# Optimization experiments

Hardware: AMD Instinct MI355X
Metric: run time of the kernel (lower is better)

## Reference

```python
import jax, jax.numpy as jnp
import numpy as np
from jax.scipy.linalg import expm

S = 64          # alphabet size (codons)
M = 8           # number of models, prod(model_shape)
N_LEAVES = 32   # leaves of the balanced binary tree
N_EDGES = 62    # nodes 0..62, every non-root node has one parent edge (edge id == child node id)
B = 1024        # batch (alignment columns)
# per-level ranges of child-node ids; node 32+j has children (2j, 2j+1), etc.
LEVELS = [(0, 32), (32, 48), (48, 56), (56, 60), (60, 62)]


def inv_stereographic_projection(p):
    # maps R^{s-1} -> unit sphere S^{s-1}
    n2 = jnp.sum(p * p, axis=-1, keepdims=True)
    return jnp.concatenate([2.0 * p / (n2 + 1.0), (n2 - 1.0) / (n2 + 1.0)], axis=-1)


def generator(R, pi):
    # R: (M, s(s-1)/2) exchangeabilities, pi: (M, s) stationary distribution
    iu, ju = np.triu_indices(S, 1)
    A = jnp.zeros((M, S, S), R.dtype).at[:, iu, ju].set(R).at[:, ju, iu].set(R)
    Q = A * pi[:, None, :]                       # Q_ij = A_ij * pi_j (off-diagonal)
    row = jnp.sum(Q, axis=-1)                    # (M, S)
    return Q - jnp.eye(S, dtype=Q.dtype) * row[:, :, None]


def felsenstein(leave_configuration, R_inv, pi_inv, lengths):
    pi = inv_stereographic_projection(pi_inv) ** 2           # (M, S), rows sum to 1
    R = jnp.exp(R_inv)                                       # positive rates
    Q = generator(R, pi)                                     # (M, S, S)
    tQ = lengths[:, None, None, None] * Q[None]              # (E, M, S, S)
    P = jax.vmap(expm)(tQ.reshape(-1, S, S)).reshape(N_EDGES, M, S, S)
    # leaf alphas: tile leaf observations over the M models -> (n_leaves, B, M, S)
    prev = jnp.broadcast_to(
        leave_configuration.transpose(1, 0, 2)[:, :, None, :],
        (N_LEAVES, leave_configuration.shape[0], M, S))
    # level-synchronous pruning: messages up each parent edge, then product of the two children
    for a, b in LEVELS:
        msg = jnp.einsum('emcd,ebmd->ebmc', P[a:b], prev)    # per-edge transition
        prev = msg[0::2] * msg[1::2]                         # combine sibling pairs
    root = prev[0]                                           # (B, M, S)
    out = jnp.einsum('bms,ms->bm', root, pi)                 # P(data | model m)
    return out.reshape(out.shape[0], M)                      # (B, *model_shape)


def setup_inputs() -> dict:
    key = jax.random.key(0)
    k1, k2, k3, k4 = jax.random.split(key, 4)
    leave_configuration = jax.random.uniform(k1, (B, N_LEAVES, S), dtype=jnp.float32)
    tree_indices = jnp.zeros((B,), dtype=jnp.int32)          # single tree (F=1)
    R_inv = jax.random.uniform(k2, (M, S * (S - 1) // 2), dtype=jnp.float32,
                               minval=-1.0, maxval=1.0)
    pi_inv = jnp.full((M, S - 1), 1.0 / (np.sqrt(S) - 1.0), dtype=jnp.float32) \
        + 0.01 * jax.random.normal(k3, (M, S - 1), dtype=jnp.float32)
    lengths = jax.random.uniform(k4, (N_EDGES,), dtype=jnp.float32,
                                 minval=0.05, maxval=0.5)
    return {'leave_configuration': leave_configuration, 'R_inv': R_inv,
            'pi_inv': pi_inv, 'lengths': lengths, 'tree_indices': tree_indices}


def reference(leave_configuration, R_inv, pi_inv, lengths, tree_indices):
    # F=1: tf.dynamic_partition/gather_nd batch slicing is the identity, so
    # tree_indices is closed over / unused.
    return felsenstein(leave_configuration, R_inv, pi_inv, lengths)
```

## Files before the change

kernel.cpp:

```cpp
#include <hip/hip_runtime.h>

typedef unsigned short u16;
typedef unsigned int u32;
typedef __attribute__((ext_vector_type(8))) __bf16 bf16x8;
typedef __attribute__((ext_vector_type(4))) float f32x4;

constexpr size_t OFF_PI  = 0;
constexpr size_t OFF_PBH = 512;
constexpr size_t OFF_PBL = OFF_PBH + 1015808;

union FR { uint4 u; bf16x8 v; };

__device__ __forceinline__ void split_bf16(float x, u16& h, u16& l) {
  u32 b = __float_as_uint(x);
  u32 hb = (b + 0x7fffu + ((b >> 16) & 1u)) & 0xffff0000u;
  h = (u16)(hb >> 16);
  float r = x - __uint_as_float(hb);
  l = (u16)(__float_as_uint(r) >> 16);
}

__device__ __forceinline__ void split8(const f32x4 a, const f32x4 b,
                                       uint4& hi, uint4& lo) {
  u16 h[8], l[8];
  split_bf16(a.x, h[0], l[0]); split_bf16(a.y, h[1], l[1]);
  split_bf16(a.z, h[2], l[2]); split_bf16(a.w, h[3], l[3]);
  split_bf16(b.x, h[4], l[4]); split_bf16(b.y, h[5], l[5]);
  split_bf16(b.z, h[6], l[6]); split_bf16(b.w, h[7], l[7]);
  hi.x = h[0] | ((u32)h[1] << 16); hi.y = h[2] | ((u32)h[3] << 16);
  hi.z = h[4] | ((u32)h[5] << 16); hi.w = h[6] | ((u32)h[7] << 16);
  lo.x = l[0] | ((u32)l[1] << 16); lo.y = l[2] | ((u32)l[3] << 16);
  lo.z = l[4] | ((u32)l[5] << 16); lo.w = l[6] | ((u32)l[7] << 16);
}

__device__ __forceinline__ void mfma3(f32x4& a, const uint4 ah, const uint4 al,
                                      const uint4 bh, const uint4 bl) {
  FR Ah, Al, Bh, Bl;
  Ah.u = ah; Al.u = al; Bh.u = bh; Bl.u = bl;
  a = __builtin_amdgcn_mfma_f32_16x16x32_bf16(Ah.v, Bh.v, a, 0, 0, 0);
  a = __builtin_amdgcn_mfma_f32_16x16x32_bf16(Ah.v, Bl.v, a, 0, 0, 0);
  a = __builtin_amdgcn_mfma_f32_16x16x32_bf16(Al.v, Bh.v, a, 0, 0, 0);
}

__device__ __forceinline__ void xt_read2(const u32* b, int row, int chunk,
                                         uint4& hi, uint4& lo) {
  const int dw = (row << 5) + (((chunk + row) & 7) << 2);
  hi = *(const uint4*)&b[dw];
  lo = *(const uint4*)&b[2048 + dw];
}
__device__ __forceinline__ void xt_write4(u32* b, int row, int cp, int half,
                                          const f32x4 v) {
  u16 h[4], l[4];
  split_bf16(v.x, h[0], l[0]); split_bf16(v.y, h[1], l[1]);
  split_bf16(v.z, h[2], l[2]); split_bf16(v.w, h[3], l[3]);
  const int dw = (row << 5) + (((cp + row) & 7) << 2) + half * 2;
  uint2 hh, ll;
  hh.x = h[0] | ((u32)h[1] << 16); hh.y = h[2] | ((u32)h[3] << 16);
  ll.x = l[0] | ((u32)l[1] << 16); ll.y = l[2] | ((u32)l[3] << 16);
  *(uint2*)&b[dw] = hh;
  *(uint2*)&b[2048 + dw] = ll;
}

__global__ __launch_bounds__(1024) void k_pcomb(
    const float* __restrict__ R_inv, const float* __restrict__ pi_inv,
    const float* __restrict__ lengths, float* __restrict__ ws,
    u16* __restrict__ PBH, u16* __restrict__ PBL) {
  const int m = blockIdx.x & 7, prt = blockIdx.x >> 3;
  const int tid = threadIdx.x, lane = tid & 63, w = tid >> 6;
  const int ln = lane & 15, kq = lane >> 4;
  const int ct = w >> 2, bt = w & 3;
  __shared__ float pis[64];
  __shared__ float n2s;
  __shared__ __align__(16) float Qs[64 * 68];
  __shared__ __align__(16) u32 PB[7][4096];

  if (tid < 64) {
    float p = (tid < 63) ? pi_inv[m * 63 + tid] : 0.f;
    float v = p * p;
    #pragma unroll
    for (int off = 32; off; off >>= 1) v += __shfl_down(v, off, 64);
    if (tid == 0) n2s = v;
  }
  __syncthreads();
  if (tid < 64) {
    const float den = n2s + 1.f;
    const float x = (tid < 63) ? 2.f * pi_inv[m * 63 + tid] / den
                               : (n2s - 1.f) / den;
    const float pv = x * x;
    pis[tid] = pv;
    if (prt == 0) ws[OFF_PI + (size_t)m * 64 + tid] = pv;
  }
  __syncthreads();
  for (int idx = tid; idx < 4096; idx += 1024) {
    const int i = idx >> 6, j = idx & 63;
    float q = 0.f;
    if (i != j) {
      const int a = min(i, j), b = max(i, j);
      const int kk = a * (127 - a) / 2 + (b - a - 1);
      q = expf(R_inv[m * 2016 + kk]) * pis[j];
    }
    Qs[i * 68 + j] = q;
  }
  __syncthreads();
  if (tid < 64) {
    float s = 0.f;
    #pragma unroll 4
    for (int j4 = 0; j4 < 64; j4 += 4) {
      const f32x4 q = *(const f32x4*)&Qs[tid * 68 + j4];
      s += q.x + q.y + q.z + q.w;
    }
    Qs[tid * 68 + tid] = -s;
  }
  __syncthreads();
  float q[12][4];
  #pragma unroll
  for (int r = 0; r < 4; ++r) q[0][r] = Qs[(ct * 16 + kq * 4 + r) * 68 + bt * 16 + ln];
  if (tid < 512) {
    const int i = tid >> 3, c = tid & 7;
    const f32x4 a = *(const f32x4*)&Qs[i * 68 + c * 8];
    const f32x4 b = *(const f32x4*)&Qs[i * 68 + c * 8 + 4];
    uint4 h, l;
    split8(a, b, h, l);
    const int dw = (i << 5) + (((c + i) & 7) << 2);
    *(uint4*)&PB[0][dw] = h;
    *(uint4*)&PB[0][2048 + dw] = l;
  } else {
    const int t2 = tid - 512, j = t2 >> 3, c = t2 & 7;
    f32x4 a, b;
    a.x = Qs[(c * 8 + 0) * 68 + j]; a.y = Qs[(c * 8 + 1) * 68 + j];
    a.z = Qs[(c * 8 + 2) * 68 + j]; a.w = Qs[(c * 8 + 3) * 68 + j];
    b.x = Qs[(c * 8 + 4) * 68 + j]; b.y = Qs[(c * 8 + 5) * 68 + j];
    b.z = Qs[(c * 8 + 6) * 68 + j]; b.w = Qs[(c * 8 + 7) * 68 + j];
    uint4 h, l;
    split8(a, b, h, l);
    const int dw = (j << 5) + (((c + j) & 7) << 2);
    *(uint4*)&PB[3][dw] = h;
    *(uint4*)&PB[3][2048 + dw] = l;
  }
  __syncthreads();

  const f32x4 z = {0.f, 0.f, 0.f, 0.f};
  auto mmstep = [&](const u32* RX, const u32* CY, float* qk, u32* dstC,
                    u32* dstR) {
    uint4 ah[2], al[2], bh[2], bl[2];
    #pragma unroll
    for (int kh = 0; kh < 2; ++kh) {
      xt_read2(RX, ct * 16 + ln, kh * 4 + kq, ah[kh], al[kh]);
      xt_read2(CY, bt * 16 + ln, kh * 4 + kq, bh[kh], bl[kh]);
    }
    f32x4 a = z;
    #pragma unroll
    for (int kh = 0; kh < 2; ++kh) mfma3(a, ah[kh], al[kh], bh[kh], bl[kh]);
    #pragma unroll
    for (int r = 0; r < 4; ++r) qk[r] = a[r];
    if (dstC) xt_write4(dstC, bt * 16 + ln, 2 * ct + (kq >> 1), kq & 1, a);
    if (dstR) {
      #pragma unroll
      for (int kh = 0; kh < 2; ++kh) {
        xt_read2(CY, ct * 16 + ln, kh * 4 + kq, ah[kh], al[kh]);
        xt_read2(RX, bt * 16 + ln, kh * 4 + kq, bh[kh], bl[kh]);
      }
      f32x4 a2 = z;
      #pragma unroll
      for (int kh = 0; kh < 2; ++kh) mfma3(a2, ah[kh], al[kh], bh[kh], bl[kh]);
      xt_write4(dstR, bt * 16 + ln, 2 * ct + (kq >> 1), kq & 1, a2);
    }
  };
  mmstep(PB[0], PB[3], q[1], PB[4], PB[1]);  __syncthreads();
  mmstep(PB[1], PB[3], q[2], PB[5], nullptr); __syncthreads();
  mmstep(PB[1], PB[4], q[3], PB[6], PB[2]);  __syncthreads();
  mmstep(PB[2], PB[3], q[4], nullptr, nullptr);
  mmstep(PB[2], PB[4], q[5], nullptr, nullptr);
  mmstep(PB[2], PB[5], q[6], nullptr, nullptr);
  mmstep(PB[2], PB[6], q[7], nullptr, PB[0]); __syncthreads();
  mmstep(PB[0], PB[3], q[8], nullptr, nullptr);
  mmstep(PB[0], PB[4], q[9], nullptr, nullptr);
  mmstep(PB[0], PB[5], q[10], nullptr, nullptr);
  mmstep(PB[0], PB[6], q[11], nullptr, nullptr);

  #pragma unroll
  for (int ei = 0; ei < 2; ++ei) {
    const int e = prt * 2 + ei;
    if (e >= 62) break;
    const float t = lengths[e];
    const int jcol = bt * 16 + ln;
    float av[4];
    #pragma unroll
    for (int r = 0; r < 4; ++r)
      av[r] = (ct * 16 + kq * 4 + r == jcol) ? 1.f : 0.f;
    float cf = 1.f;
    #pragma unroll
    for (int k = 1; k <= 12; ++k) {
      cf *= t / (float)k;
      #pragma unroll
      for (int r = 0; r < 4; ++r) av[r] = fmaf(cf, q[k - 1][r], av[r]);
    }
    const size_t base = (((size_t)e * 8 + m) << 12) + jcol;
    #pragma unroll
    for (int r = 0; r < 4; ++r) {
      u16 h, l;
      split_bf16(av[r], h, l);
      const size_t o = base + (size_t)(ct * 16 + kq * 4 + r) * 64;
      PBH[o] = h;
      PBL[o] = l;
    }
  }
}

#define SE(e, i0, i1, o) \
  ((u32)(e) | ((u32)(i0) << 8) | ((u32)(i1) << 16) | ((u32)(o) << 24))
__device__ const u32 SCHED[31] = {
    SE(0, 0, 0, 0),  SE(2, 0, 0, 1),  SE(4, 0, 0, 2),  SE(6, 0, 0, 3),
    SE(32, 0, 1, 4), SE(34, 2, 3, 5), SE(8, 0, 0, 6),  SE(10, 0, 0, 7),
    SE(36, 6, 7, 8), SE(12, 0, 0, 0), SE(14, 0, 0, 1), SE(16, 0, 0, 2),
    SE(38, 0, 1, 3), SE(48, 4, 5, 6), SE(18, 0, 0, 7),
    SE(40, 2, 7, 0), SE(50, 8, 3, 1), SE(20, 0, 0, 4), SE(22, 0, 0, 5),
    SE(42, 4, 5, 2), SE(24, 0, 0, 3), SE(26, 0, 0, 7), SE(56, 6, 1, 8),
    SE(52, 0, 2, 1), SE(44, 3, 7, 4), SE(28, 0, 0, 5), SE(30, 0, 0, 6),
    SE(46, 5, 6, 0),
    SE(54, 4, 0, 2),
    SE(58, 1, 2, 3),
    SE(60, 8, 3, 15)};
__device__ const int PH[12] = {0, 4, 8, 12, 15, 19, 23, 27, 28, 29, 30, 31};

__global__ __launch_bounds__(512, 4) void k_tree(
    const float* __restrict__ leaves, const u16* __restrict__ Phi,
    const u16* __restrict__ Plo, const float* __restrict__ ws,
    float* __restrict__ out) {
  const int m = blockIdx.x & 7, btile = blockIdx.x >> 3;
  const int tid = threadIdx.x, lane = tid & 63, w = tid >> 6;
  const int ln = lane & 15, kq = lane >> 4;
  const int ct0 = (w & 1) * 2;
  __shared__ __align__(16) u32 slots[9 * 2048];
  __shared__ float psum[2][4][16];
  const f32x4 z = {0.f, 0.f, 0.f, 0.f};
  f32x4 rootp[2][2] = {{z, z}, {z, z}};

  for (int ph = 0; ph < 11; ++ph) {
    const int p0 = PH[ph], np = PH[ph + 1] - p0;
    const int pi = w >> 1;
    if (pi < np) {
      const u32 d = SCHED[p0 + pi];
      const int e0 = d & 0xff, i0 = (d >> 8) & 0xff, i1 = (d >> 16) & 0xff,
                os = d >> 24;
      f32x4 acc[2][2];
      #pragma unroll
      for (int s = 0; s < 2; ++s) {
        uint4 bh[2][2], bl[2][2];
        if (e0 < 32) {
          #pragma unroll
          for (int bi = 0; bi < 2; ++bi) {
            const int row = bi * 16 + ln;
            #pragma unroll
            for (int kh = 0; kh < 2; ++kh) {
              const float* g = leaves + (size_t)(btile * 32 + row) * 2048 +
                               (size_t)(e0 + s) * 64 + kh * 32 + kq * 8;
              const f32x4 xa = *(const f32x4*)g;
              const f32x4 xb = *(const f32x4*)(g + 4);
              split8(xa, xb, bh[bi][kh], bl[bi][kh]);
            }
          }
        } else {
          const u32* nb0 = &slots[(s ? i1 : i0) * 2048];
          #pragma unroll
          for (int bi = 0; bi < 2; ++bi) {
            const int row = bi * 16 + ln;
            const u32* nb = nb0 + row * 64;
            #pragma unroll
            for (int kh = 0; kh < 2; ++kh) {
              const int jc = kh * 8 + kq * 2;
              const uint4 A = *(const uint4*)&nb[((jc + row) & 15) << 2];
              const uint4 B = *(const uint4*)&nb[((jc + 1 + row) & 15) << 2];
              bh[bi][kh].x = A.x; bh[bi][kh].y = A.y;
              bh[bi][kh].z = B.x; bh[bi][kh].w = B.y;
              bl[bi][kh].x = A.z; bl[bi][kh].y = A.w;
              bl[bi][kh].z = B.z; bl[bi][kh].w = B.w;
            }
          }
        }
        uint4 pfh[2][2], pfl[2][2];
        const size_t pb = ((size_t)(e0 + s) * 8 + m) << 12;
        #pragma unroll
        for (int ci = 0; ci < 2; ++ci)
          #pragma unroll
          for (int kh = 0; kh < 2; ++kh) {
            const size_t off =
                pb + (size_t)((ct0 + ci) * 16 + ln) * 64 + kh * 32 + kq * 8;
            pfh[ci][kh] = *(const uint4*)(Phi + off);
            pfl[ci][kh] = *(const uint4*)(Plo + off);
          }
        #pragma unroll
        for (int ci = 0; ci < 2; ++ci)
          #pragma unroll
          for (int bi = 0; bi < 2; ++bi) {
            f32x4 a = z;
            #pragma unroll
            for (int kh = 0; kh < 2; ++kh)
              mfma3(a, pfh[ci][kh], pfl[ci][kh], bh[bi][kh], bl[bi][kh]);
            if (s == 0) {
              acc[ci][bi] = a;
            } else {
              const f32x4 pr = acc[ci][bi] * a;
              if (os == 15) {
                rootp[ci][bi] = pr;
              } else {
                u16 h[4], l[4];
                split_bf16(pr.x, h[0], l[0]); split_bf16(pr.y, h[1], l[1]);
                split_bf16(pr.z, h[2], l[2]); split_bf16(pr.w, h[3], l[3]);
                uint4 pk;
                pk.x = h[0] | ((u32)h[1] << 16); pk.y = h[2] | ((u32)h[3] << 16);
                pk.z = l[0] | ((u32)l[1] << 16); pk.w = l[2] | ((u32)l[3] << 16);
                const int row = bi * 16 + ln;
                const int jc = (ct0 + ci) * 4 + kq;
                *(uint4*)&slots[os * 2048 + row * 64 +
                                (((jc + row) & 15) << 2)] = pk;
              }
            }
          }
      }
    }
    __syncthreads();
  }
  if (w < 2) {
    #pragma unroll
    for (int ci = 0; ci < 2; ++ci) {
      const int ct = ct0 + ci;
      const f32x4 piv =
          *(const f32x4*)&ws[OFF_PI + (size_t)m * 64 + ct * 16 + kq * 4];
      #pragma unroll
      for (int bi = 0; bi < 2; ++bi) {
        const f32x4 pr = rootp[ci][bi];
        float v = pr.x * piv.x + pr.y * piv.y + pr.z * piv.z + pr.w * piv.w;
        v += __shfl_xor(v, 16, 64);
        v += __shfl_xor(v, 32, 64);
        if (lane < 16) psum[bi][ct][lane] = v;
      }
    }
  }
  __syncthreads();
  if (tid < 32) {
    const int bi = tid >> 4, bb = tid & 15;
    out[(size_t)(btile * 32 + tid) * 8 + m] =
        psum[bi][0][bb] + psum[bi][1][bb] + psum[bi][2][bb] + psum[bi][3][bb];
  }
}

extern "C" void kernel_launch(void* const* d_in, const int* in_sizes, int n_in,
                              void* d_out, int out_size, void* d_ws, size_t ws_size,
                              hipStream_t stream) {
  const float* leaves  = (const float*)d_in[0];
  const float* R_inv   = (const float*)d_in[1];
  const float* pi_inv  = (const float*)d_in[2];
  const float* lengths = (const float*)d_in[3];
  float* out = (float*)d_out;
  float* ws  = (float*)d_ws;

  u16* PBH = (u16*)(ws + OFF_PBH);
  u16* PBL = (u16*)(ws + OFF_PBL);

  hipLaunchKernelGGL(k_pcomb, dim3(256), dim3(1024), 0, stream, R_inv, pi_inv,
                     lengths, ws, PBH, PBL);
  hipLaunchKernelGGL(k_tree, dim3(256), dim3(512), 0, stream, leaves, PBH, PBL,
                     ws, out);
}
```

Before: 127.6 us.

## Split tree kernel into wide leaf-level kernel plus upper-level kernel

Replaces the single fused tree kernel, which walked the whole tree per 32-column tile on 256 blocks, with two kernels. A leaf-level kernel on 2048 blocks computes all leaf-pair products and writes the parent nodes as hi/lo bf16 to a workspace. An upper-level kernel on 512 blocks of 16 columns then reduces the remaining levels in shared memory. The aim is more parallelism and occupancy for the dominant leaf level, paid for with an extra launch and a global round trip of the intermediate node vectors.

```diff
diff --git a/kernel.cpp b/kernel.cpp
--- a/kernel.cpp
+++ b/kernel.cpp
@@ -8,6 +8,8 @@
 constexpr size_t OFF_PI  = 0;
 constexpr size_t OFF_PBH = 512;
 constexpr size_t OFF_PBL = OFF_PBH + 1015808;
+constexpr size_t OFF_NDH = OFF_PBL + 1015808;
+constexpr size_t OFF_NDL = OFF_NDH + 4194304;
 
 union FR { uint4 u; bf16x8 v; };
 
@@ -113,7 +115,8 @@
   __syncthreads();
   float q[12][4];
   #pragma unroll
-  for (int r = 0; r < 4; ++r) q[0][r] = Qs[(ct * 16 + kq * 4 + r) * 68 + bt * 16 + ln];
+  for (int r = 0; r < 4; ++r)
+    q[0][r] = Qs[(ct * 16 + kq * 4 + r) * 68 + bt * 16 + ln];
   if (tid < 512) {
     const int i = tid >> 3, c = tid & 7;
     const f32x4 a = *(const f32x4*)&Qs[i * 68 + c * 8];
@@ -206,142 +209,170 @@
   }
 }
 
-#define SE(e, i0, i1, o) \
-  ((u32)(e) | ((u32)(i0) << 8) | ((u32)(i1) << 16) | ((u32)(o) << 24))
-__device__ const u32 SCHED[31] = {
-    SE(0, 0, 0, 0),  SE(2, 0, 0, 1),  SE(4, 0, 0, 2),  SE(6, 0, 0, 3),
-    SE(32, 0, 1, 4), SE(34, 2, 3, 5), SE(8, 0, 0, 6),  SE(10, 0, 0, 7),
-    SE(36, 6, 7, 8), SE(12, 0, 0, 0), SE(14, 0, 0, 1), SE(16, 0, 0, 2),
-    SE(38, 0, 1, 3), SE(48, 4, 5, 6), SE(18, 0, 0, 7),
-    SE(40, 2, 7, 0), SE(50, 8, 3, 1), SE(20, 0, 0, 4), SE(22, 0, 0, 5),
-    SE(42, 4, 5, 2), SE(24, 0, 0, 3), SE(26, 0, 0, 7), SE(56, 6, 1, 8),
-    SE(52, 0, 2, 1), SE(44, 3, 7, 4), SE(28, 0, 0, 5), SE(30, 0, 0, 6),
-    SE(46, 5, 6, 0),
-    SE(54, 4, 0, 2),
-    SE(58, 1, 2, 3),
-    SE(60, 8, 3, 15)};
-__device__ const int PH[12] = {0, 4, 8, 12, 15, 19, 23, 27, 28, 29, 30, 31};
-
-__global__ __launch_bounds__(512, 4) void k_tree(
+__global__ __launch_bounds__(256) void k_L0(
     const float* __restrict__ leaves, const u16* __restrict__ Phi,
-    const u16* __restrict__ Plo, const float* __restrict__ ws,
-    float* __restrict__ out) {
-  const int m = blockIdx.x & 7, btile = blockIdx.x >> 3;
+    const u16* __restrict__ Plo, u16* __restrict__ NDH,
+    u16* __restrict__ NDL) {
+  const int blk = blockIdx.x;
+  const int m = blk & 7, p = (blk >> 3) & 15, jt = blk >> 7;
   const int tid = threadIdx.x, lane = tid & 63, w = tid >> 6;
   const int ln = lane & 15, kq = lane >> 4;
-  const int ct0 = (w & 1) * 2;
-  __shared__ __align__(16) u32 slots[9 * 2048];
-  __shared__ float psum[2][4][16];
+  const int b = jt * 64 + w * 16 + ln;
   const f32x4 z = {0.f, 0.f, 0.f, 0.f};
-  f32x4 rootp[2][2] = {{z, z}, {z, z}};
-
-  for (int ph = 0; ph < 11; ++ph) {
-    const int p0 = PH[ph], np = PH[ph + 1] - p0;
-    const int pi = w >> 1;
-    if (pi < np) {
-      const u32 d = SCHED[p0 + pi];
-      const int e0 = d & 0xff, i0 = (d >> 8) & 0xff, i1 = (d >> 16) & 0xff,
-                os = d >> 24;
-      f32x4 acc[2][2];
-      #pragma unroll
-      for (int s = 0; s < 2; ++s) {
-        uint4 bh[2][2], bl[2][2];
-        if (e0 < 32) {
-          #pragma unroll
-          for (int bi = 0; bi < 2; ++bi) {
-            const int row = bi * 16 + ln;
-            #pragma unroll
-            for (int kh = 0; kh < 2; ++kh) {
-              const float* g = leaves + (size_t)(btile * 32 + row) * 2048 +
-                               (size_t)(e0 + s) * 64 + kh * 32 + kq * 8;
-              const f32x4 xa = *(const f32x4*)g;
-              const f32x4 xb = *(const f32x4*)(g + 4);
-              split8(xa, xb, bh[bi][kh], bl[bi][kh]);
-            }
-          }
+  f32x4 acc0[4], acc1[4];
+
+  #pragma unroll
+  for (int s = 0; s < 2; ++s) {
+    uint4 bh[2], bl[2];
+    #pragma unroll
+    for (int kh = 0; kh < 2; ++kh) {
+      const float* g = leaves + (size_t)b * 2048 + (size_t)(2 * p + s) * 64 +
+                       kh * 32 + kq * 8;
+      const f32x4 xa = *(const f32x4*)g;
+      const f32x4 xb = *(const f32x4*)(g + 4);
+      split8(xa, xb, bh[kh], bl[kh]);
+    }
+    const size_t pb = ((size_t)(2 * p + s) * 8 + m) << 12;
+    f32x4* acc = s ? acc1 : acc0;
+    #pragma unroll
+    for (int ci = 0; ci < 4; ++ci) {
+      f32x4 a = z;
+      #pragma unroll
+      for (int kh = 0; kh < 2; ++kh) {
+        const size_t off = pb + (size_t)(ci * 16 + ln) * 64 + kh * 32 + kq * 8;
+        const uint4 pah = *(const uint4*)(Phi + off);
+        const uint4 pal = *(const uint4*)(Plo + off);
+        mfma3(a, pah, pal, bh[kh], bl[kh]);
+      }
+      acc[ci] = a;
+    }
+  }
+  const size_t nb = (((size_t)p * 8 + m) << 16) + (size_t)b * 64;
+  #pragma unroll
+  for (int ci = 0; ci < 4; ++ci) {
+    const f32x4 pr = acc0[ci] * acc1[ci];
+    u16 h[4], l[4];
+    split_bf16(pr.x, h[0], l[0]); split_bf16(pr.y, h[1], l[1]);
+    split_bf16(pr.z, h[2], l[2]); split_bf16(pr.w, h[3], l[3]);
+    ushort4 h4, l4;
+    h4.x = h[0]; h4.y = h[1]; h4.z = h[2]; h4.w = h[3];
+    l4.x = l[0]; l4.y = l[1]; l4.z = l[2]; l4.w = l[3];
+    const size_t o = nb + ci * 16 + kq * 4;
+    *(ushort4*)(NDH + o) = h4;
+    *(ushort4*)(NDL + o) = l4;
+  }
+}
+
+__global__ __launch_bounds__(512) void k_upper(
+    const u16* __restrict__ NDH, const u16* __restrict__ NDL,
+    const u16* __restrict__ Phi, const u16* __restrict__ Plo,
+    const float* __restrict__ ws, float* __restrict__ out) {
+  const int m = blockIdx.x & 7, jt = blockIdx.x >> 3;
+  const int tid = threadIdx.x, lane = tid & 63, w = tid >> 6;
+  const int ln = lane & 15, kq = lane >> 4;
+  __shared__ __align__(16) u32 slots[12 * 1024];
+  __shared__ float psum[4][16];
+  const f32x4 z = {0.f, 0.f, 0.f, 0.f};
+
+  auto node_read = [&](int slot, int row, int kh, uint4& bh, uint4& bl) {
+    const int jc = kh * 8 + kq * 2;
+    const u32* nb = &slots[slot * 1024 + row * 64];
+    const uint4 A = *(const uint4*)&nb[((jc + row) & 15) << 2];
+    const uint4 B = *(const uint4*)&nb[((jc + 1 + row) & 15) << 2];
+    bh.x = A.x; bh.y = A.y; bh.z = B.x; bh.w = B.y;
+    bl.x = A.z; bl.y = A.w; bl.z = B.z; bl.w = B.w;
+  };
+  auto node_write = [&](int slot, int row, int jc, const f32x4 v) {
+    u16 h[4], l[4];
+    split_bf16(v.x, h[0], l[0]); split_bf16(v.y, h[1], l[1]);
+    split_bf16(v.z, h[2], l[2]); split_bf16(v.w, h[3], l[3]);
+    uint4 pk;
+    pk.x = h[0] | ((u32)h[1] << 16); pk.y = h[2] | ((u32)h[3] << 16);
+    pk.z = l[0] | ((u32)l[1] << 16); pk.w = l[2] | ((u32)l[3] << 16);
+    *(uint4*)&slots[slot * 1024 + row * 64 + (((jc + row) & 15) << 2)] = pk;
+  };
+
+  auto do_pair = [&](int e0, int g0, int s0, int s1, int outSlot, int ct0,
+                     int nct, bool fromGlobal, f32x4* rootout) {
+    uint4 bh[2][2], bl[2][2];
+    #pragma unroll
+    for (int s = 0; s < 2; ++s)
+      #pragma unroll
+      for (int kh = 0; kh < 2; ++kh) {
+        if (fromGlobal) {
+          const size_t nb =
+              (((size_t)(g0 + s) * 8 + m) << 16) + (size_t)(jt * 16 + ln) * 64;
+          bh[s][kh] = *(const uint4*)(NDH + nb + kh * 32 + kq * 8);
+          bl[s][kh] = *(const uint4*)(NDL + nb + kh * 32 + kq * 8);
         } else {
-          const u32* nb0 = &slots[(s ? i1 : i0) * 2048];
-          #pragma unroll
-          for (int bi = 0; bi < 2; ++bi) {
-            const int row = bi * 16 + ln;
-            const u32* nb = nb0 + row * 64;
-            #pragma unroll
-            for (int kh = 0; kh < 2; ++kh) {
-              const int jc = kh * 8 + kq * 2;
-              const uint4 A = *(const uint4*)&nb[((jc + row) & 15) << 2];
-              const uint4 B = *(const uint4*)&nb[((jc + 1 + row) & 15) << 2];
-              bh[bi][kh].x = A.x; bh[bi][kh].y = A.y;
-              bh[bi][kh].z = B.x; bh[bi][kh].w = B.y;
-              bl[bi][kh].x = A.z; bl[bi][kh].y = A.w;
-              bl[bi][kh].z = B.z; bl[bi][kh].w = B.w;
-            }
+          node_read(s ? s1 : s0, ln, kh, bh[s][kh], bl[s][kh]);
+        }
+      }
+    f32x4 acc0[4];
+    #pragma unroll
+    for (int s = 0; s < 2; ++s) {
+      const size_t pb = ((size_t)(e0 + s) * 8 + m) << 12;
+      #pragma unroll
+      for (int ci = 0; ci < 4; ++ci) {
+        if (ci >= nct) continue;
+        uint4 pah[2], pal[2];
+        #pragma unroll
+        for (int kh = 0; kh < 2; ++kh) {
+          const size_t off =
+              pb + (size_t)((ct0 + ci) * 16 + ln) * 64 + kh * 32 + kq * 8;
+          pah[kh] = *(const uint4*)(Phi + off);
+          pal[kh] = *(const uint4*)(Plo + off);
+        }
+        f32x4 a = z;
+        #pragma unroll
+        for (int kh = 0; kh < 2; ++kh)
+          mfma3(a, pah[kh], pal[kh], bh[s][kh], bl[s][kh]);
+        if (s == 0) {
+          acc0[ci] = a;
+        } else {
+          const f32x4 pr = acc0[ci] * a;
+          if (rootout) {
+            rootout[ci] = pr;
+          } else {
+            node_write(outSlot, ln, (ct0 + ci) * 4 + kq, pr);
           }
         }
-        uint4 pfh[2][2], pfl[2][2];
-        const size_t pb = ((size_t)(e0 + s) * 8 + m) << 12;
-        #pragma unroll
-        for (int ci = 0; ci < 2; ++ci)
-          #pragma unroll
-          for (int kh = 0; kh < 2; ++kh) {
-            const size_t off =
-                pb + (size_t)((ct0 + ci) * 16 + ln) * 64 + kh * 32 + kq * 8;
-            pfh[ci][kh] = *(const uint4*)(Phi + off);
-            pfl[ci][kh] = *(const uint4*)(Plo + off);
-          }
-        #pragma unroll
-        for (int ci = 0; ci < 2; ++ci)
-          #pragma unroll
-          for (int bi = 0; bi < 2; ++bi) {
-            f32x4 a = z;
-            #pragma unroll
-            for (int kh = 0; kh < 2; ++kh)
-              mfma3(a, pfh[ci][kh], pfl[ci][kh], bh[bi][kh], bl[bi][kh]);
-            if (s == 0) {
-              acc[ci][bi] = a;
-            } else {
-              const f32x4 pr = acc[ci][bi] * a;
-              if (os == 15) {
-                rootp[ci][bi] = pr;
-              } else {
-                u16 h[4], l[4];
-                split_bf16(pr.x, h[0], l[0]); split_bf16(pr.y, h[1], l[1]);
-                split_bf16(pr.z, h[2], l[2]); split_bf16(pr.w, h[3], l[3]);
-                uint4 pk;
-                pk.x = h[0] | ((u32)h[1] << 16); pk.y = h[2] | ((u32)h[3] << 16);
-                pk.z = l[0] | ((u32)l[1] << 16); pk.w = l[2] | ((u32)l[3] << 16);
-                const int row = bi * 16 + ln;
-                const int jc = (ct0 + ci) * 4 + kq;
-                *(uint4*)&slots[os * 2048 + row * 64 +
-                                (((jc + row) & 15) << 2)] = pk;
-              }
-            }
-          }
       }
     }
-    __syncthreads();
-  }
+  };
+
+  do_pair(32 + 2 * w, 2 * w, -1, -1, w, 0, 4, true, nullptr);
+  __syncthreads();
+  {
+    const int j = w >> 1, ch = (w & 1) * 2;
+    do_pair(48 + 2 * j, 0, 2 * j, 2 * j + 1, 8 + j, ch, 2, false, nullptr);
+  }
+  __syncthreads();
+  if (w < 4) {
+    const int j = w >> 1, ch = (w & 1) * 2;
+    do_pair(56 + 2 * j, 0, 8 + 2 * j, 8 + 2 * j + 1, j, ch, 2, false, nullptr);
+  }
+  __syncthreads();
   if (w < 2) {
+    f32x4 root[4];
+    const int ch = w * 2;
+    do_pair(60, 0, 0, 1, -1, ch, 2, false, root);
     #pragma unroll
     for (int ci = 0; ci < 2; ++ci) {
-      const int ct = ct0 + ci;
+      const int ct = ch + ci;
       const f32x4 piv =
           *(const f32x4*)&ws[OFF_PI + (size_t)m * 64 + ct * 16 + kq * 4];
-      #pragma unroll
-      for (int bi = 0; bi < 2; ++bi) {
-        const f32x4 pr = rootp[ci][bi];
-        float v = pr.x * piv.x + pr.y * piv.y + pr.z * piv.z + pr.w * piv.w;
-        v += __shfl_xor(v, 16, 64);
-        v += __shfl_xor(v, 32, 64);
-        if (lane < 16) psum[bi][ct][lane] = v;
-      }
-    }
-  }
-  __syncthreads();
-  if (tid < 32) {
-    const int bi = tid >> 4, bb = tid & 15;
-    out[(size_t)(btile * 32 + tid) * 8 + m] =
-        psum[bi][0][bb] + psum[bi][1][bb] + psum[bi][2][bb] + psum[bi][3][bb];
-  }
+      const f32x4 pr = root[ci];
+      float v = pr.x * piv.x + pr.y * piv.y + pr.z * piv.z + pr.w * piv.w;
+      v += __shfl_xor(v, 16, 64);
+      v += __shfl_xor(v, 32, 64);
+      if (lane < 16) psum[ct][lane] = v;
+    }
+  }
+  __syncthreads();
+  if (tid < 16)
+    out[(size_t)(jt * 16 + tid) * 8 + m] =
+        psum[0][tid] + psum[1][tid] + psum[2][tid] + psum[3][tid];
 }
 
 extern "C" void kernel_launch(void* const* d_in, const int* in_sizes, int n_in,
@@ -356,9 +387,13 @@
 
   u16* PBH = (u16*)(ws + OFF_PBH);
   u16* PBL = (u16*)(ws + OFF_PBL);
+  u16* NDH = (u16*)(ws + OFF_NDH);
+  u16* NDL = (u16*)(ws + OFF_NDL);
 
   hipLaunchKernelGGL(k_pcomb, dim3(256), dim3(1024), 0, stream, R_inv, pi_inv,
                      lengths, ws, PBH, PBL);
-  hipLaunchKernelGGL(k_tree, dim3(256), dim3(512), 0, stream, leaves, PBH, PBL,
-                     ws, out);
-}
+  hipLaunchKernelGGL(k_L0, dim3(2048), dim3(256), 0, stream, leaves, PBH, PBL,
+                     NDH, NDL);
+  hipLaunchKernelGGL(k_upper, dim3(512), dim3(512), 0, stream, NDH, NDL, PBH,
+                     PBL, ws, out);
+}
```

Result: slower. 152.2 us (+19.3%).
